# Kernel tuning notes

Measured on AMD Instinct MI355X. Metric: run time of the kernel, lower is better.

The kernel has to match this reference:

```python
import jax, jax.numpy as jnp
import numpy as np

EPS = 1e-5


def _ligru_layer(x, W, U, gamma, beta):
    """One bidirectional LiGRU layer. x: (B,T,F) -> (B,T,2H)."""
    B = x.shape[0]
    H = U.shape[1]
    # bidirectional: stack forward copy and time-flipped copy along batch
    x2 = jnp.concatenate([x, x[:, ::-1]], axis=0)  # (2B, T, F)
    w = jnp.einsum('btf,gf->btg', x2, W)           # (2B, T, 2H)
    # training-mode BatchNorm1d over flattened (2B*T, 2H), biased variance
    flat = w.reshape(-1, w.shape[-1])
    mean = flat.mean(axis=0)
    var = flat.var(axis=0)
    w = (w - mean) * jax.lax.rsqrt(var + EPS) * gamma + beta

    def step(h, wt):
        gates = wt + h @ U.T            # (2B, 2H)
        at, zt = gates[:, :H], gates[:, H:]
        z = jax.nn.sigmoid(zt)
        h = z * h + (1.0 - z) * jax.nn.relu(at)
        return h, h

    h0 = jnp.zeros((w.shape[0], H), dtype=w.dtype)
    _, hs = jax.lax.scan(step, h0, jnp.swapaxes(w, 0, 1))  # (T, 2B, H)
    hs = jnp.swapaxes(hs, 0, 1)                            # (2B, T, H)
    h_f, h_b = hs[:B], hs[B:, ::-1]                        # un-flip backward dir
    return jnp.concatenate([h_f, h_b], axis=2)             # (B, T, 2H)


def setup_inputs() -> dict:
    key = jax.random.key(0)
    ks = jax.random.split(key, 9)
    B, T, F, H = 16, 500, 512, 1024
    return {
        'x': jax.random.normal(ks[0], (B, T, F), jnp.float32),
        'w0': jax.random.normal(ks[1], (2 * H, F), jnp.float32) * (1.0 / np.sqrt(F)),
        'u0': jax.random.normal(ks[2], (2 * H, H), jnp.float32) * (1.0 / np.sqrt(H)),
        'g0': jax.random.uniform(ks[3], (2 * H,), jnp.float32, 0.5, 1.5),
        'b0': jax.random.normal(ks[4], (2 * H,), jnp.float32) * 0.1,
        'w1': jax.random.normal(ks[5], (2 * H, 2 * H), jnp.float32) * (1.0 / np.sqrt(2 * H)),
        'u1': jax.random.normal(ks[6], (2 * H, H), jnp.float32) * (1.0 / np.sqrt(H)),
        'g1': jax.random.uniform(ks[7], (2 * H,), jnp.float32, 0.5, 1.5),
        'b1': jax.random.normal(ks[8], (2 * H,), jnp.float32) * 0.1,
    }


def reference(x, w0, u0, g0, b0, w1, u1, g1, b1):
    h = _ligru_layer(x, w0, u0, g0, b0)   # (B, T, 2H)
    h = _ligru_layer(h, w1, u1, g1, b1)   # (B, T, 2H)
    return h
```

## Files before the change

kernel.cpp:

```cpp
#include <hip/hip_runtime.h>
#include <stdint.h>

#define KT 500
#define KH 1024
#define KG 2048
#define FPAD 16

typedef short bf16x8 __attribute__((ext_vector_type(8)));
typedef float f32x4 __attribute__((ext_vector_type(4)));

__device__ __forceinline__ unsigned short f2bf(float f){
  union { float f; unsigned int i; } u; u.f = f;
  unsigned int x = u.i;
  return (unsigned short)((x + 0x7fffu + ((x >> 16) & 1u)) >> 16);
}
__device__ __forceinline__ float bf2f(unsigned short h){
  union { unsigned int i; float f; } u; u.i = ((unsigned int)h) << 16;
  return u.f;
}

template<int OFF>
__device__ __forceinline__ void load_b128_dev_off(uint4& dst, const void* p){
  asm volatile("global_load_dwordx4 %0, %1, off offset:%c2 sc1"
               : "=v"(dst) : "v"(p), "i"(OFF) : "memory");
}
__device__ __forceinline__ void store_b32_dev(void* p, unsigned int v){
  asm volatile("global_store_dword %0, %1, off sc1"
               :: "v"(p), "v"(v) : "memory");
}
__device__ __forceinline__ void wait_vm0(){
  asm volatile("s_waitcnt vmcnt(0)" ::: "memory");
}
__device__ __forceinline__ void wait_vm8(){
  asm volatile("s_waitcnt vmcnt(8)" ::: "memory");
}

__global__ __launch_bounds__(256) void castk(const float* __restrict__ s,
                                             unsigned short* __restrict__ d, int n4){
  int i = blockIdx.x*256 + threadIdx.x;
  if (i >= n4) return;
  float4 v = ((const float4*)s)[i];
  unsigned int lo = (unsigned int)f2bf(v.x) | ((unsigned int)f2bf(v.y) << 16);
  unsigned int hi = (unsigned int)f2bf(v.z) | ((unsigned int)f2bf(v.w) << 16);
  ((uint2*)d)[i] = make_uint2(lo, hi);
}

template<int MODE, int KDIM>
__global__ __launch_bounds__(256) void gemm_bn(
    const unsigned short* __restrict__ A,
    const unsigned short* __restrict__ Bw,
    unsigned short* __restrict__ Wout)
{
  __shared__ __attribute__((aligned(16))) unsigned short As[128*72];
  __shared__ __attribute__((aligned(16))) unsigned short Bs[128*72];
  const int tid = threadIdx.x;
  const int lane = tid & 63, wid = tid >> 6;
  const int ntile = blockIdx.x, mtile = blockIdx.y;
  const int arow_loc = tid >> 3;
  const int k8 = tid & 7;

  long abaseLo[4], abaseHi[4], bbase[4];
  #pragma unroll
  for (int i = 0; i < 4; i++){
    int r = mtile*128 + i*32 + arow_loc;
    int s = r / KT;
    int t = r - s*KT;
    if (MODE == 0){
      abaseLo[i] = (s < 16) ? (long)((s*KT + t)*512)
                            : (long)(((s-16)*KT + (KT-1-t))*512);
      abaseHi[i] = 0;
    } else {
      int sp = s & 15;
      int rev = (s >= 16);
      abaseLo[i] = (long)((sp*KT + (rev ? KT-1-t : t)) * KH);
      abaseHi[i] = (long)(((16+sp)*KT + (rev ? t : KT-1-t)) * KH);
    }
    bbase[i] = (long)(ntile*128 + i*32 + arow_loc) * KDIM;
  }

  f32x4 acc[4][4];
  #pragma unroll
  for (int a=0;a<4;a++)
    #pragma unroll
    for (int b=0;b<4;b++)
      acc[a][b] = (f32x4){0.f,0.f,0.f,0.f};

  const int mhalf = wid & 1, nhalf = wid >> 1;
  const int lrow = lane & 15, quad = lane >> 4;

  for (int k0 = 0; k0 < KDIM; k0 += 64){
    const int kel = k0 + k8*8;
    #pragma unroll
    for (int i = 0; i < 4; i++){
      long aoff;
      if (MODE == 0) aoff = abaseLo[i] + kel;
      else           aoff = (kel < KH) ? (abaseLo[i] + kel) : (abaseHi[i] + (kel - KH));
      uint4 va = *(const uint4*)(A + aoff);
      uint4 vb = *(const uint4*)(Bw + bbase[i] + kel);
      *(uint4*)&As[(i*32 + arow_loc)*72 + k8*8] = va;
      *(uint4*)&Bs[(i*32 + arow_loc)*72 + k8*8] = vb;
    }
    __syncthreads();
    #pragma unroll
    for (int kk = 0; kk < 64; kk += 32){
      bf16x8 af[4], bfr[4];
      #pragma unroll
      for (int mt=0; mt<4; mt++)
        af[mt] = *(const bf16x8*)&As[(mhalf*64 + mt*16 + lrow)*72 + kk + quad*8];
      #pragma unroll
      for (int nt=0; nt<4; nt++)
        bfr[nt] = *(const bf16x8*)&Bs[(nhalf*64 + nt*16 + lrow)*72 + kk + quad*8];
      #pragma unroll
      for (int mt=0; mt<4; mt++)
        #pragma unroll
        for (int nt=0; nt<4; nt++)
          acc[mt][nt] = __builtin_amdgcn_mfma_f32_16x16x32_bf16(af[mt], bfr[nt], acc[mt][nt], 0, 0, 0);
    }
    __syncthreads();
  }

  #pragma unroll
  for (int mt=0; mt<4; mt++)
    #pragma unroll
    for (int nt=0; nt<4; nt++)
      #pragma unroll
      for (int r=0; r<4; r++){
        int grow = mtile*128 + mhalf*64 + mt*16 + quad*4 + r;
        int gcol = ntile*128 + nhalf*64 + nt*16 + lrow;
        Wout[(long)grow*KG + gcol] = f2bf(acc[mt][nt][r]);
      }
}

__global__ __launch_bounds__(256) void bn_partial(const unsigned short* __restrict__ W,
                                                  float* __restrict__ part){
  const int blk = blockIdx.x, tid = threadIdx.x;
  const int c0 = tid*8;
  float s[8], qq[8];
  #pragma unroll
  for (int j=0;j<8;j++){ s[j]=0.f; qq[j]=0.f; }
  const unsigned short* base = W + (long)blk*128*KG + c0;
  for (int r=0;r<128;r++){
    uint4 v = *(const uint4*)(base + (long)r*KG);
    unsigned int w[4] = {v.x, v.y, v.z, v.w};
    #pragma unroll
    for (int p=0;p<4;p++){
      union { unsigned int i; float f; } lo, hi;
      lo.i = w[p] << 16;
      hi.i = w[p] & 0xffff0000u;
      s[2*p]   += lo.f; qq[2*p]   += lo.f*lo.f;
      s[2*p+1] += hi.f; qq[2*p+1] += hi.f*hi.f;
    }
  }
  float* pd = part + (long)blk*4096;
  #pragma unroll
  for (int j=0;j<8;j++){ pd[c0+j] = s[j]; pd[KG + c0 + j] = qq[j]; }
}

__global__ __launch_bounds__(256) void bn_final(const float* __restrict__ part,
                                                const float* __restrict__ gamma,
                                                const float* __restrict__ beta,
                                                float* __restrict__ scsh){
  int g = blockIdx.x*256 + threadIdx.x;
  float s=0.f, qq=0.f;
  for (int b=0;b<125;b++){ s += part[(long)b*4096 + g]; qq += part[(long)b*4096 + KG + g]; }
  float mean = s * (1.f/16000.f);
  float var  = qq * (1.f/16000.f) - mean*mean;
  float sc = gamma[g] * rsqrtf(var + 1e-5f);
  scsh[g]      = sc;
  scsh[KG + g] = beta[g] - mean*sc;
}

template<int LAYER>
__global__ __launch_bounds__(256, 1) void recur(
    const unsigned short* __restrict__ Ub,
    const unsigned short* __restrict__ Wn,
    const float* __restrict__ scsh,
    unsigned short* __restrict__ hbuf,
    int* __restrict__ flags,
    unsigned short* __restrict__ hsOut,
    float* __restrict__ out)
{
  __shared__ float gA0[2][32*20];
  __shared__ float gZ0[2][32*20];
  __shared__ float gA1[2][32*20];
  __shared__ float gZ1[2][32*20];

  const int tid = threadIdx.x;
  const int q = blockIdx.x;
  const int ga = q*16;
  const int lane = tid & 63, wid = tid >> 6;
  const int lrow = lane & 15, quad = lane >> 4;
  const int m = wid & 1, kh = wid >> 1;
  const int es = tid >> 3, ep = tid & 7;

  bf16x8 ufA[16], ufZ[16];
  {
    const unsigned short* ua = Ub + (long)(ga + lrow)*KH + kh*512 + quad*8;
    const unsigned short* uz = ua + (long)KH*KH;
    #pragma unroll
    for (int c=0;c<16;c++){
      ufA[c] = *(const bf16x8*)(ua + c*32);
      asm volatile("" : "+a"(ufA[c]));
      ufZ[c] = *(const bf16x8*)(uz + c*32);
      asm volatile("" : "+a"(ufZ[c]));
    }
  }

  float2 scav = *(const float2*)&scsh[ga + 2*ep];
  float2 shav = *(const float2*)&scsh[KG + ga + 2*ep];
  float2 sczv = *(const float2*)&scsh[KH + ga + 2*ep];
  float2 shzv = *(const float2*)&scsh[KG + KH + ga + 2*ep];
  float2 hprev = make_float2(0.f, 0.f);

  const long aoff = (long)(m*16 + lrow)*KH + kh*512 + quad*8;
  const unsigned short* hb0 = hbuf + aoff;
  const unsigned short* hb1 = hbuf + 32768 + aoff;

  const int pp = kh*32 + (lane >> 1);
  const int pw = 2*m + (lane & 1);
  const int* fpoll = &flags[((pp*4 + pw)) << 4];

  for (int t = 0; t < KT; t++){
    const unsigned short* wr = Wn + (long)(es*KT + t)*KG + ga + 2*ep;
    unsigned int wa01 = *(const unsigned int*)(wr);
    unsigned int wz01 = *(const unsigned int*)(wr + KH);
    asm volatile("" ::: "memory");

    if (t > 0){
      while (__hip_atomic_load(fpoll, __ATOMIC_RELAXED,
                               __HIP_MEMORY_SCOPE_AGENT) < t){}
    } else {
      wait_vm0();
    }

    const unsigned short* hb = (t & 1) ? hb1 : hb0;
    uint4 af[16];
    #define LDAF(i) load_b128_dev_off<(i)*64>(af[i], hb)
    LDAF(0);  LDAF(1);  LDAF(2);  LDAF(3);
    LDAF(4);  LDAF(5);  LDAF(6);  LDAF(7);
    LDAF(8);  LDAF(9);  LDAF(10); LDAF(11);
    LDAF(12); LDAF(13); LDAF(14); LDAF(15);
    #undef LDAF

    f32x4 aA0 = (f32x4){0,0,0,0}, aA1 = aA0, aZ0 = aA0, aZ1 = aA0;

    wait_vm8();
    __builtin_amdgcn_sched_barrier(0);
    #pragma unroll
    for (int c=0;c<8;c+=2){
      bf16x8 x0 = *(bf16x8*)&af[c];
      bf16x8 x1 = *(bf16x8*)&af[c+1];
      aA0 = __builtin_amdgcn_mfma_f32_16x16x32_bf16(x0, ufA[c],   aA0, 0,0,0);
      aZ0 = __builtin_amdgcn_mfma_f32_16x16x32_bf16(x0, ufZ[c],   aZ0, 0,0,0);
      aA1 = __builtin_amdgcn_mfma_f32_16x16x32_bf16(x1, ufA[c+1], aA1, 0,0,0);
      aZ1 = __builtin_amdgcn_mfma_f32_16x16x32_bf16(x1, ufZ[c+1], aZ1, 0,0,0);
    }
    wait_vm0();
    __builtin_amdgcn_sched_barrier(0);
    #pragma unroll
    for (int c=8;c<16;c+=2){
      bf16x8 x0 = *(bf16x8*)&af[c];
      bf16x8 x1 = *(bf16x8*)&af[c+1];
      aA0 = __builtin_amdgcn_mfma_f32_16x16x32_bf16(x0, ufA[c],   aA0, 0,0,0);
      aZ0 = __builtin_amdgcn_mfma_f32_16x16x32_bf16(x0, ufZ[c],   aZ0, 0,0,0);
      aA1 = __builtin_amdgcn_mfma_f32_16x16x32_bf16(x1, ufA[c+1], aA1, 0,0,0);
      aZ1 = __builtin_amdgcn_mfma_f32_16x16x32_bf16(x1, ufZ[c+1], aZ1, 0,0,0);
    }
    f32x4 accA = aA0 + aA1;
    f32x4 accZ = aZ0 + aZ1;

    const int par = t & 1;
    {
      float* gAd = kh ? gA1[par] : gA0[par];
      float* gZd = kh ? gZ1[par] : gZ0[par];
      #pragma unroll
      for (int r=0;r<4;r++){
        gAd[(m*16 + quad*4 + r)*20 + lrow] = accA[r];
        gZd[(m*16 + quad*4 + r)*20 + lrow] = accZ[r];
      }
    }
    __syncthreads();

    float2 va0 = *(const float2*)&gA0[par][es*20 + 2*ep];
    float2 va1 = *(const float2*)&gA1[par][es*20 + 2*ep];
    float2 vz0 = *(const float2*)&gZ0[par][es*20 + 2*ep];
    float2 vz1 = *(const float2*)&gZ1[par][es*20 + 2*ep];
    float aa0 = va0.x + va1.x + bf2f((unsigned short)(wa01 & 0xffff)) * scav.x + shav.x;
    float aa1 = va0.y + va1.y + bf2f((unsigned short)(wa01 >> 16))    * scav.y + shav.y;
    float zz0 = vz0.x + vz1.x + bf2f((unsigned short)(wz01 & 0xffff)) * sczv.x + shzv.x;
    float zz1 = vz0.y + vz1.y + bf2f((unsigned short)(wz01 >> 16))    * sczv.y + shzv.y;
    float z0 = 1.f/(1.f + __expf(-zz0));
    float z1 = 1.f/(1.f + __expf(-zz1));
    float hn0 = z0*hprev.x + (1.f - z0)*fmaxf(aa0, 0.f);
    float hn1 = z1*hprev.y + (1.f - z1)*fmaxf(aa1, 0.f);
    hprev = make_float2(hn0, hn1);

    unsigned int hpack = (unsigned int)f2bf(hn0) | ((unsigned int)f2bf(hn1) << 16);

    store_b32_dev(hbuf + ((t+1)&1)*32768 + es*KH + ga + 2*ep, hpack);
    if (LAYER == 0){
      *(unsigned int*)&hsOut[(long)(es*KT + t)*KH + ga + 2*ep] = hpack;
    } else {
      if (es < 16)
        *(float2*)&out[(long)(es*KT + t)*KG + ga + 2*ep] = make_float2(hn0, hn1);
      else
        *(float2*)&out[(long)((es-16)*KT + (KT-1-t))*KG + KH + ga + 2*ep] = make_float2(hn0, hn1);
    }

    wait_vm0();
    if (lane == 0)
      __hip_atomic_store(&flags[(q*4 + wid) << 4], t + 1, __ATOMIC_RELAXED,
                         __HIP_MEMORY_SCOPE_AGENT);
  }
}

extern "C" void kernel_launch(void* const* d_in, const int* in_sizes, int n_in,
                              void* d_out, int out_size, void* d_ws, size_t ws_size,
                              hipStream_t stream)
{
  const float* x  = (const float*)d_in[0];
  const float* w0 = (const float*)d_in[1];
  const float* u0 = (const float*)d_in[2];
  const float* g0 = (const float*)d_in[3];
  const float* b0 = (const float*)d_in[4];
  const float* w1 = (const float*)d_in[5];
  const float* u1 = (const float*)d_in[6];
  const float* g1 = (const float*)d_in[7];
  const float* b1 = (const float*)d_in[8];
  float* out = (float*)d_out;

  char* p = (char*)d_ws;
  auto alloc = [&](size_t n){ char* r = p; p += (n + 255) & ~(size_t)255; return r; };
  unsigned short* xb   = (unsigned short*)alloc((size_t)16*KT*512*2);
  unsigned short* w0b  = (unsigned short*)alloc((size_t)KG*512*2);
  unsigned short* u0b  = (unsigned short*)alloc((size_t)KG*KH*2);
  unsigned short* w1b  = (unsigned short*)alloc((size_t)KG*KG*2);
  unsigned short* u1b  = (unsigned short*)alloc((size_t)KG*KH*2);
  unsigned short* wbuf = (unsigned short*)alloc((size_t)32*KT*KG*2);
  unsigned short* hs0  = (unsigned short*)alloc((size_t)32*KT*KH*2);
  float* part          = (float*)alloc((size_t)125*4096*4);
  float* scsh          = (float*)alloc((size_t)2*KG*4);
  unsigned short* hbuf = (unsigned short*)alloc((size_t)2*2*32*KH*2);
  int* flags           = (int*)alloc((size_t)2*64*4*FPAD*4);

  auto cast = [&](const float* s, unsigned short* d, int n){
    int n4 = n >> 2;
    castk<<<(n4+255)/256, 256, 0, stream>>>(s, d, n4);
  };
  cast(x,  xb,  16*KT*512);
  cast(w0, w0b, KG*512);
  cast(u0, u0b, KG*KH);
  cast(w1, w1b, KG*KG);
  cast(u1, u1b, KG*KH);
  hipMemsetAsync(hbuf,  0, (size_t)2*2*32*KH*2, stream);
  hipMemsetAsync(flags, 0, (size_t)2*64*4*FPAD*4, stream);

  gemm_bn<0,512><<<dim3(16,125), 256, 0, stream>>>(xb, w0b, wbuf);
  bn_partial<<<125,256,0,stream>>>(wbuf, part);
  bn_final<<<8,256,0,stream>>>(part, g0, b0, scsh);
  recur<0><<<64,256,0,stream>>>(u0b, wbuf, scsh, hbuf, flags, hs0, (float*)nullptr);

  gemm_bn<1,2048><<<dim3(16,125), 256, 0, stream>>>(hs0, w1b, wbuf);
  bn_partial<<<125,256,0,stream>>>(wbuf, part);
  bn_final<<<8,256,0,stream>>>(part, g1, b1, scsh);
  recur<1><<<64,256,0,stream>>>(u1b, wbuf, scsh, hbuf + 2*32*KH, flags + 64*4*FPAD,
                                (unsigned short*)nullptr, out);
}
```

Before: 4.304 ms.

## Use time-indexed hidden-state history with per-step counter barrier instead of double buffer

The recurrence now writes each step's hidden state into a full time-indexed history buffer (T x 32 x H), which doubles as the layer-0 output in a time-major layout that the layer-1 GEMM reads. Synchronisation moves from polling per-wave flags to polling one atomic counter per timestep that all 256 waves increment. The h loads also drop the sc1 cache-coherence bit. This removes the separate hsOut store and the double-buffer reuse hazard, and skips the t=0 matmul. In exchange, all waves contend on one atomic per step, and loads without sc1 risk reading stale data from non-coherent caches.

```diff
diff --git a/kernel.cpp b/kernel.cpp
--- a/kernel.cpp
+++ b/kernel.cpp
@@ -20,8 +20,8 @@
 }
 
 template<int OFF>
-__device__ __forceinline__ void load_b128_dev_off(uint4& dst, const void* p){
-  asm volatile("global_load_dwordx4 %0, %1, off offset:%c2 sc1"
+__device__ __forceinline__ void load_b128_l2(uint4& dst, const void* p){
+  asm volatile("global_load_dwordx4 %0, %1, off offset:%c2"
                : "=v"(dst) : "v"(p), "i"(OFF) : "memory");
 }
 __device__ __forceinline__ void store_b32_dev(void* p, unsigned int v){
@@ -72,8 +72,8 @@
     } else {
       int sp = s & 15;
       int rev = (s >= 16);
-      abaseLo[i] = (long)((sp*KT + (rev ? KT-1-t : t)) * KH);
-      abaseHi[i] = (long)(((16+sp)*KT + (rev ? t : KT-1-t)) * KH);
+      abaseLo[i] = (long)(((rev ? KT-1-t : t)*32 + sp) * KH);
+      abaseHi[i] = (long)(((rev ? t : KT-1-t)*32 + 16 + sp) * KH);
     }
     bbase[i] = (long)(ntile*128 + i*32 + arow_loc) * KDIM;
   }
@@ -175,9 +175,8 @@
     const unsigned short* __restrict__ Ub,
     const unsigned short* __restrict__ Wn,
     const float* __restrict__ scsh,
-    unsigned short* __restrict__ hbuf,
+    unsigned short* __restrict__ hx,
     int* __restrict__ flags,
-    unsigned short* __restrict__ hsOut,
     float* __restrict__ out)
 {
   __shared__ float gA0[2][32*20];
@@ -212,13 +211,7 @@
   float2 shzv = *(const float2*)&scsh[KG + KH + ga + 2*ep];
   float2 hprev = make_float2(0.f, 0.f);
 
-  const long aoff = (long)(m*16 + lrow)*KH + kh*512 + quad*8;
-  const unsigned short* hb0 = hbuf + aoff;
-  const unsigned short* hb1 = hbuf + 32768 + aoff;
-
-  const int pp = kh*32 + (lane >> 1);
-  const int pw = 2*m + (lane & 1);
-  const int* fpoll = &flags[((pp*4 + pw)) << 4];
+  const long lbase = (long)(m*16 + lrow)*KH + kh*512 + quad*8;
 
   for (int t = 0; t < KT; t++){
     const unsigned short* wr = Wn + (long)(es*KT + t)*KG + ga + 2*ep;
@@ -226,48 +219,52 @@
     unsigned int wz01 = *(const unsigned int*)(wr + KH);
     asm volatile("" ::: "memory");
 
+    f32x4 accA, accZ;
     if (t > 0){
-      while (__hip_atomic_load(fpoll, __ATOMIC_RELAXED,
-                               __HIP_MEMORY_SCOPE_AGENT) < t){}
+      while (__hip_atomic_load(&flags[(t-1)*FPAD], __ATOMIC_RELAXED,
+                               __HIP_MEMORY_SCOPE_AGENT) < 256){}
+      asm volatile("" ::: "memory");
+
+      const unsigned short* hb = hx + (long)(t-1)*32*KH + lbase;
+      uint4 af[16];
+      #define LDAF(i) load_b128_l2<(i)*64>(af[i], hb)
+      LDAF(0);  LDAF(1);  LDAF(2);  LDAF(3);
+      LDAF(4);  LDAF(5);  LDAF(6);  LDAF(7);
+      LDAF(8);  LDAF(9);  LDAF(10); LDAF(11);
+      LDAF(12); LDAF(13); LDAF(14); LDAF(15);
+      #undef LDAF
+
+      f32x4 aA0 = (f32x4){0,0,0,0}, aA1 = aA0, aZ0 = aA0, aZ1 = aA0;
+
+      wait_vm8();
+      __builtin_amdgcn_sched_barrier(0);
+      #pragma unroll
+      for (int c=0;c<8;c+=2){
+        bf16x8 x0 = *(bf16x8*)&af[c];
+        bf16x8 x1 = *(bf16x8*)&af[c+1];
+        aA0 = __builtin_amdgcn_mfma_f32_16x16x32_bf16(x0, ufA[c],   aA0, 0,0,0);
+        aZ0 = __builtin_amdgcn_mfma_f32_16x16x32_bf16(x0, ufZ[c],   aZ0, 0,0,0);
+        aA1 = __builtin_amdgcn_mfma_f32_16x16x32_bf16(x1, ufA[c+1], aA1, 0,0,0);
+        aZ1 = __builtin_amdgcn_mfma_f32_16x16x32_bf16(x1, ufZ[c+1], aZ1, 0,0,0);
+      }
+      wait_vm0();
+      __builtin_amdgcn_sched_barrier(0);
+      #pragma unroll
+      for (int c=8;c<16;c+=2){
+        bf16x8 x0 = *(bf16x8*)&af[c];
+        bf16x8 x1 = *(bf16x8*)&af[c+1];
+        aA0 = __builtin_amdgcn_mfma_f32_16x16x32_bf16(x0, ufA[c],   aA0, 0,0,0);
+        aZ0 = __builtin_amdgcn_mfma_f32_16x16x32_bf16(x0, ufZ[c],   aZ0, 0,0,0);
+        aA1 = __builtin_amdgcn_mfma_f32_16x16x32_bf16(x1, ufA[c+1], aA1, 0,0,0);
+        aZ1 = __builtin_amdgcn_mfma_f32_16x16x32_bf16(x1, ufZ[c+1], aZ1, 0,0,0);
+      }
+      accA = aA0 + aA1;
+      accZ = aZ0 + aZ1;
     } else {
       wait_vm0();
-    }
-
-    const unsigned short* hb = (t & 1) ? hb1 : hb0;
-    uint4 af[16];
-    #define LDAF(i) load_b128_dev_off<(i)*64>(af[i], hb)
-    LDAF(0);  LDAF(1);  LDAF(2);  LDAF(3);
-    LDAF(4);  LDAF(5);  LDAF(6);  LDAF(7);
-    LDAF(8);  LDAF(9);  LDAF(10); LDAF(11);
-    LDAF(12); LDAF(13); LDAF(14); LDAF(15);
-    #undef LDAF
-
-    f32x4 aA0 = (f32x4){0,0,0,0}, aA1 = aA0, aZ0 = aA0, aZ1 = aA0;
-
-    wait_vm8();
-    __builtin_amdgcn_sched_barrier(0);
-    #pragma unroll
-    for (int c=0;c<8;c+=2){
-      bf16x8 x0 = *(bf16x8*)&af[c];
-      bf16x8 x1 = *(bf16x8*)&af[c+1];
-      aA0 = __builtin_amdgcn_mfma_f32_16x16x32_bf16(x0, ufA[c],   aA0, 0,0,0);
-      aZ0 = __builtin_amdgcn_mfma_f32_16x16x32_bf16(x0, ufZ[c],   aZ0, 0,0,0);
-      aA1 = __builtin_amdgcn_mfma_f32_16x16x32_bf16(x1, ufA[c+1], aA1, 0,0,0);
-      aZ1 = __builtin_amdgcn_mfma_f32_16x16x32_bf16(x1, ufZ[c+1], aZ1, 0,0,0);
-    }
-    wait_vm0();
-    __builtin_amdgcn_sched_barrier(0);
-    #pragma unroll
-    for (int c=8;c<16;c+=2){
-      bf16x8 x0 = *(bf16x8*)&af[c];
-      bf16x8 x1 = *(bf16x8*)&af[c+1];
-      aA0 = __builtin_amdgcn_mfma_f32_16x16x32_bf16(x0, ufA[c],   aA0, 0,0,0);
-      aZ0 = __builtin_amdgcn_mfma_f32_16x16x32_bf16(x0, ufZ[c],   aZ0, 0,0,0);
-      aA1 = __builtin_amdgcn_mfma_f32_16x16x32_bf16(x1, ufA[c+1], aA1, 0,0,0);
-      aZ1 = __builtin_amdgcn_mfma_f32_16x16x32_bf16(x1, ufZ[c+1], aZ1, 0,0,0);
-    }
-    f32x4 accA = aA0 + aA1;
-    f32x4 accZ = aZ0 + aZ1;
+      accA = (f32x4){0,0,0,0};
+      accZ = (f32x4){0,0,0,0};
+    }
 
     const int par = t & 1;
     {
@@ -297,20 +294,17 @@
 
     unsigned int hpack = (unsigned int)f2bf(hn0) | ((unsigned int)f2bf(hn1) << 16);
 
-    store_b32_dev(hbuf + ((t+1)&1)*32768 + es*KH + ga + 2*ep, hpack);
-    if (LAYER == 0){
-      *(unsigned int*)&hsOut[(long)(es*KT + t)*KH + ga + 2*ep] = hpack;
-    } else {
+    store_b32_dev(hx + (long)t*32*KH + (long)es*KH + ga + 2*ep, hpack);
+    wait_vm0();
+    if (lane == 0)
+      atomicAdd(&flags[t*FPAD], 1);
+
+    if (LAYER == 1){
       if (es < 16)
         *(float2*)&out[(long)(es*KT + t)*KG + ga + 2*ep] = make_float2(hn0, hn1);
       else
         *(float2*)&out[(long)((es-16)*KT + (KT-1-t))*KG + KH + ga + 2*ep] = make_float2(hn0, hn1);
     }
-
-    wait_vm0();
-    if (lane == 0)
-      __hip_atomic_store(&flags[(q*4 + wid) << 4], t + 1, __ATOMIC_RELAXED,
-                         __HIP_MEMORY_SCOPE_AGENT);
   }
 }
 
@@ -337,11 +331,10 @@
   unsigned short* w1b  = (unsigned short*)alloc((size_t)KG*KG*2);
   unsigned short* u1b  = (unsigned short*)alloc((size_t)KG*KH*2);
   unsigned short* wbuf = (unsigned short*)alloc((size_t)32*KT*KG*2);
-  unsigned short* hs0  = (unsigned short*)alloc((size_t)32*KT*KH*2);
+  unsigned short* hs0  = (unsigned short*)alloc((size_t)KT*32*KH*2);
   float* part          = (float*)alloc((size_t)125*4096*4);
   float* scsh          = (float*)alloc((size_t)2*KG*4);
-  unsigned short* hbuf = (unsigned short*)alloc((size_t)2*2*32*KH*2);
-  int* flags           = (int*)alloc((size_t)2*64*4*FPAD*4);
+  int* flags           = (int*)alloc((size_t)2*KT*FPAD*4);
 
   auto cast = [&](const float* s, unsigned short* d, int n){
     int n4 = n >> 2;
@@ -352,17 +345,15 @@
   cast(u0, u0b, KG*KH);
   cast(w1, w1b, KG*KG);
   cast(u1, u1b, KG*KH);
-  hipMemsetAsync(hbuf,  0, (size_t)2*2*32*KH*2, stream);
-  hipMemsetAsync(flags, 0, (size_t)2*64*4*FPAD*4, stream);
+  hipMemsetAsync(flags, 0, (size_t)2*KT*FPAD*4, stream);
 
   gemm_bn<0,512><<<dim3(16,125), 256, 0, stream>>>(xb, w0b, wbuf);
   bn_partial<<<125,256,0,stream>>>(wbuf, part);
   bn_final<<<8,256,0,stream>>>(part, g0, b0, scsh);
-  recur<0><<<64,256,0,stream>>>(u0b, wbuf, scsh, hbuf, flags, hs0, (float*)nullptr);
+  recur<0><<<64,256,0,stream>>>(u0b, wbuf, scsh, hs0, flags, (float*)nullptr);
 
   gemm_bn<1,2048><<<dim3(16,125), 256, 0, stream>>>(hs0, w1b, wbuf);
   bn_partial<<<125,256,0,stream>>>(wbuf, part);
   bn_final<<<8,256,0,stream>>>(part, g1, b1, scsh);
-  recur<1><<<64,256,0,stream>>>(u1b, wbuf, scsh, hbuf + 2*32*KH, flags + 64*4*FPAD,
-                                (unsigned short*)nullptr, out);
-}
+  recur<1><<<64,256,0,stream>>>(u1b, wbuf, scsh, hs0, flags + KT*FPAD, out);
+}
```

Result: slower. 7.383 ms (+71.6%).
